# Kernel tuning notes

Measured on AMD Instinct MI355X. Metric: run time of the kernel, lower is better.

Reference implementation:

```python
import jax, jax.numpy as jnp
import numpy as np

N_NODES = 100000
N_EDGES = 1000000
D_IN = 64
D_OUT = 64


def setup_inputs() -> dict:
    key = jax.random.key(0)
    k1, k2, k3, k4, k5 = jax.random.split(key, 5)
    x = jax.random.normal(k1, (N_NODES, D_IN), dtype=jnp.float32)
    W = jax.random.normal(k2, (D_OUT, D_IN), dtype=jnp.float32) / np.sqrt(D_IN)
    edge_weights = jax.random.uniform(k3, (N_EDGES,), dtype=jnp.float32)
    source = jax.random.randint(k4, (N_EDGES,), 0, N_NODES, dtype=jnp.int64 if jax.config.read('jax_enable_x64') else jnp.int32)
    target = jax.random.randint(k5, (N_EDGES,), 0, N_NODES, dtype=jnp.int64 if jax.config.read('jax_enable_x64') else jnp.int32)
    return {"x": x, "W": W, "edge_weights": edge_weights,
            "source": source, "target": target, "num_nodes": N_NODES}


def reference(x, W, edge_weights, source, target, num_nodes):
    # Linear (no bias): h = x @ W^T, shape (num_nodes, out)
    h = jnp.einsum('nd,od->no', x, W)
    # Gather messages per edge, scale by edge weights
    msg = h[source] * edge_weights[:, None]  # (num_edges, out)
    # Scatter-add by target node (sum aggregation)
    delta = jax.ops.segment_sum(msg, target, num_segments=num_nodes)
    return delta
```

## Files before the change

### kernel.cpp

```cpp
#include <hip/hip_runtime.h>


#define D     64
#define BKT   64
#define BSH   6
#define NBMAX 2048
#define CAP   1024
#define CAPB  1024

__global__ __launch_bounds__(256) void gcn_scatter_kernel(
    const float* __restrict__ x, const float* __restrict__ ew,
    const int* __restrict__ src, const int* __restrict__ tgt,
    float* __restrict__ s, int n_edges)
{
    int lane = threadIdx.x & 63;
    int e = blockIdx.x * 4 + (threadIdx.x >> 6);
    if (e >= n_edges) return;
    int sn = src[e];
    int tn = tgt[e];
    float w = ew[e];
    float v = x[(size_t)sn * D + lane] * w;
    atomicAdd(&s[(size_t)tn * D + lane], v);
}

__global__ __launch_bounds__(256) void gcn_gemm_kernel(
    const float* __restrict__ s, const float* __restrict__ W,
    float* __restrict__ out, int n_nodes)
{
    __shared__ float4 xs[64 * 17];
    const int tid  = threadIdx.x;
    const int lane = tid & 63;
    const int wid  = __builtin_amdgcn_readfirstlane(tid >> 6);
    const int row0 = blockIdx.x * 64;

    const float4* s4 = reinterpret_cast<const float4*>(s);
#pragma unroll
    for (int k = 0; k < 4; ++k) {
        int f  = tid + k * 256;
        int r  = f >> 4;
        int c4 = f & 15;
        float4 v = make_float4(0.f, 0.f, 0.f, 0.f);
        if (row0 + r < n_nodes)
            v = s4[(size_t)(row0 + r) * 16 + c4];
        xs[r * 17 + c4] = v;
    }
    __syncthreads();

    float acc[16];
#pragma unroll
    for (int j = 0; j < 16; ++j) acc[j] = 0.f;

    const int o0 = wid * 16;
    const float4* W4 = reinterpret_cast<const float4*>(W);
#pragma unroll
    for (int d4 = 0; d4 < 16; ++d4) {
        float4 xv = xs[lane * 17 + d4];
#pragma unroll
        for (int j = 0; j < 16; ++j) {
            float4 wv = W4[(size_t)(o0 + j) * 16 + d4];
            acc[j] += xv.x * wv.x + xv.y * wv.y + xv.z * wv.z + xv.w * wv.w;
        }
    }

    const int row = row0 + lane;
    if (row < n_nodes) {
        float4* out4 = reinterpret_cast<float4*>(out);
#pragma unroll
        for (int j4 = 0; j4 < 4; ++j4) {
            float4 v = make_float4(acc[j4 * 4 + 0], acc[j4 * 4 + 1],
                                   acc[j4 * 4 + 2], acc[j4 * 4 + 3]);
            out4[(size_t)row * 16 + wid * 4 + j4] = v;
        }
    }
}

__device__ __forceinline__ unsigned f2bf(float f) {
    unsigned u = __float_as_uint(f);
    return (u + 0x7FFFu + ((u >> 16) & 1u)) >> 16;
}

__global__ __launch_bounds__(256) void convert_init_kernel(
    const float* __restrict__ x, uint2* __restrict__ xb, int n4,
    int* __restrict__ bbeg, int* __restrict__ bcur, int nb)
{
    const int g = blockIdx.x * 256 + threadIdx.x;
    if (g < nb) { bbeg[g] = g * CAPB; bcur[g] = g * CAPB; }
    const float4* x4 = reinterpret_cast<const float4*>(x);
    for (int i = g; i < n4; i += gridDim.x * 256) {
        float4 v = x4[i];
        uint2 o;
        o.x = f2bf(v.x) | (f2bf(v.y) << 16);
        o.y = f2bf(v.z) | (f2bf(v.w) << 16);
        xb[i] = o;
    }
}

__global__ __launch_bounds__(256) void convert_hist_kernel(
    const float* __restrict__ x, uint2* __restrict__ xb, int n4,
    const int* __restrict__ tgt, int* __restrict__ bcnt,
    int n_edges, int nb, int epb)
{
    __shared__ int h[NBMAX];
    const int tid = threadIdx.x;
    for (int i = tid; i < nb; i += 256) h[i] = 0;

    const float4* x4 = reinterpret_cast<const float4*>(x);
    for (int i = blockIdx.x * 256 + tid; i < n4; i += gridDim.x * 256) {
        float4 v = x4[i];
        uint2 o;
        o.x = f2bf(v.x) | (f2bf(v.y) << 16);
        o.y = f2bf(v.z) | (f2bf(v.w) << 16);
        xb[i] = o;
    }
    __syncthreads();

    const int e0 = blockIdx.x * epb;
    const int e1 = min(e0 + epb, n_edges);
    for (int e = e0 + tid; e < e1; e += 256)
        atomicAdd(&h[tgt[e] >> BSH], 1);
    __syncthreads();
    for (int b = tid; b < nb; b += 256) {
        int c = h[b];
        if (c) atomicAdd(&bcnt[b], c);
    }
}

__global__ __launch_bounds__(1024) void bucket_scan_kernel(
    const int* __restrict__ bcnt, int* __restrict__ bstarts,
    int* __restrict__ bcur, int nb, int n_edges)
{
    __shared__ int lds[1024];
    const int tid = threadIdx.x;
    const int i0 = 2 * tid, i1 = 2 * tid + 1;
    int v0 = (i0 < nb) ? bcnt[i0] : 0;
    int v1 = (i1 < nb) ? bcnt[i1] : 0;
    int tsum = v0 + v1;
    lds[tid] = tsum;
    __syncthreads();
    for (int off = 1; off < 1024; off <<= 1) {
        int a = (tid >= off) ? lds[tid - off] : 0;
        __syncthreads();
        lds[tid] += a;
        __syncthreads();
    }
    int pre = lds[tid] - tsum;
    if (i0 < nb) { bstarts[i0] = pre;      bcur[i0] = pre; }
    if (i1 < nb) { bstarts[i1] = pre + v0; bcur[i1] = pre + v0; }
    if (tid == 0) bstarts[nb] = n_edges;
}

__global__ __launch_bounds__(256) void bucket_scatter_kernel(
    const int* __restrict__ src, const int* __restrict__ tgt,
    const float* __restrict__ ew, int* __restrict__ bcur,
    int2* __restrict__ pairs, int n_edges, int nb, int epb)
{
    __shared__ int h[NBMAX];
    __shared__ int base[NBMAX];
    const int tid = threadIdx.x;
    for (int i = tid; i < nb; i += 256) h[i] = 0;
    __syncthreads();
    const int e0 = blockIdx.x * epb;
    const int e1 = min(e0 + epb, n_edges);

    for (int e = e0 + tid; e < e1; e += 256)
        atomicAdd(&h[tgt[e] >> BSH], 1);
    __syncthreads();

    for (int b = tid; b < nb; b += 256) {
        int c = h[b];
        base[b] = c ? atomicAdd(&bcur[b], c) : 0;
        h[b] = 0;
    }
    __syncthreads();

    for (int e = e0 + tid; e < e1; e += 256) {
        int t = tgt[e];
        int b = t >> BSH;
        int r = atomicAdd(&h[b], 1);
        pairs[base[b] + r] =
            make_int2(((t & (BKT - 1)) << 24) | src[e], __float_as_int(ew[e]));
    }
}

__global__ __launch_bounds__(512, 6) void bucket_sort_reduce_gemm_kernel(
    const uint2* __restrict__ xb, const float* __restrict__ W,
    const int* __restrict__ bbeg, const int* __restrict__ bend,
    const int2* __restrict__ pairs,
    float* __restrict__ out, int n_nodes, int nb)
{
    __shared__ float Wl[64 * 66];
    __shared__ int2  ep[CAP];
    __shared__ int   segIncl[BKT];
    __shared__ int   rankc[BKT];
    __shared__ float accRow[8][64];

    const int tid  = threadIdx.x;
    const int lane = tid & 63;
    const int wv   = tid >> 6;
    const int q4   = lane >> 4;
    const int m    = lane & 15;

    for (int i = tid; i < 64 * 64; i += 512)
        Wl[(i >> 6) * 66 + (i & 63)] = W[i];

    const int b   = blockIdx.x;
    const int beg = bbeg[b];
    const int end = bend[b];

    float4 acc[8];
#pragma unroll
    for (int s = 0; s < 8; ++s) acc[s] = make_float4(0.f, 0.f, 0.f, 0.f);

    for (int cbeg = beg; cbeg < end; cbeg += CAP) {
        const int ccnt = min(CAP, end - cbeg);

        int2 pr0 = make_int2(0, 0), pr1 = make_int2(0, 0);
        if (tid < ccnt)       pr0 = pairs[cbeg + tid];
        if (tid + 512 < ccnt) pr1 = pairs[cbeg + tid + 512];

        if (tid < BKT) segIncl[tid] = 0;
        __syncthreads();

        if (tid < ccnt)       atomicAdd(&segIncl[((unsigned)pr0.x) >> 24], 1);
        if (tid + 512 < ccnt) atomicAdd(&segIncl[((unsigned)pr1.x) >> 24], 1);
        __syncthreads();

        if (wv == 0) {
            int c0 = segIncl[lane];
            int v = c0;
#pragma unroll
            for (int off = 1; off < 64; off <<= 1) {
                int n = __shfl_up(v, off);
                if (lane >= off) v += n;
            }
            segIncl[lane] = v;
            rankc[lane]   = v - c0;
        }
        __syncthreads();

        if (tid < ccnt) {
            int pos = atomicAdd(&rankc[((unsigned)pr0.x) >> 24], 1);
            ep[pos] = pr0;
        }
        if (tid + 512 < ccnt) {
            int pos = atomicAdd(&rankc[((unsigned)pr1.x) >> 24], 1);
            ep[pos] = pr1;
        }
        __syncthreads();

#pragma unroll
        for (int g = 0; g < 2; ++g) {
            int e0, e1, e2, e3, x1_0, x1_1, x1_2, x1_3;
            {
                const int tl0 = (g * 4 + 0) * 8 + wv;
                const int tl1 = (g * 4 + 1) * 8 + wv;
                const int tl2 = (g * 4 + 2) * 8 + wv;
                const int tl3 = (g * 4 + 3) * 8 + wv;
                e0 = __builtin_amdgcn_readfirstlane(tl0 ? segIncl[tl0 - 1] : 0);
                e1 = __builtin_amdgcn_readfirstlane(segIncl[tl1 - 1]);
                e2 = __builtin_amdgcn_readfirstlane(segIncl[tl2 - 1]);
                e3 = __builtin_amdgcn_readfirstlane(segIncl[tl3 - 1]);
                x1_0 = __builtin_amdgcn_readfirstlane(segIncl[tl0]);
                x1_1 = __builtin_amdgcn_readfirstlane(segIncl[tl1]);
                x1_2 = __builtin_amdgcn_readfirstlane(segIncl[tl2]);
                x1_3 = __builtin_amdgcn_readfirstlane(segIncl[tl3]);
            }
            const int c1_0 = max(x1_0 - 1, 0);
            const int c1_1 = max(x1_1 - 1, 0);
            const int c1_2 = max(x1_2 - 1, 0);
            const int c1_3 = max(x1_3 - 1, 0);
            float4 a0 = acc[g * 4 + 0];
            float4 a1 = acc[g * 4 + 1];
            float4 a2 = acc[g * 4 + 2];
            float4 a3 = acc[g * 4 + 3];

            while ((e0 < x1_0) | (e1 < x1_1) | (e2 < x1_2) | (e3 < x1_3)) {
                const int ea0 = e0 + q4, ea1 = e1 + q4;
                const int ea2 = e2 + q4, ea3 = e3 + q4;
                int2 p0 = ep[min(ea0, c1_0)];
                int2 p1 = ep[min(ea1, c1_1)];
                int2 p2 = ep[min(ea2, c1_2)];
                int2 p3 = ep[min(ea3, c1_3)];
                uint2 r0 = xb[(size_t)(p0.x & 0xFFFFFF) * 16 + m];
                uint2 r1 = xb[(size_t)(p1.x & 0xFFFFFF) * 16 + m];
                uint2 r2 = xb[(size_t)(p2.x & 0xFFFFFF) * 16 + m];
                uint2 r3 = xb[(size_t)(p3.x & 0xFFFFFF) * 16 + m];
                float w0 = (ea0 < x1_0) ? __int_as_float(p0.y) : 0.f;
                float w1 = (ea1 < x1_1) ? __int_as_float(p1.y) : 0.f;
                float w2 = (ea2 < x1_2) ? __int_as_float(p2.y) : 0.f;
                float w3 = (ea3 < x1_3) ? __int_as_float(p3.y) : 0.f;
                a0.x += w0 * __uint_as_float(r0.x << 16);
                a0.y += w0 * __uint_as_float(r0.x & 0xFFFF0000u);
                a0.z += w0 * __uint_as_float(r0.y << 16);
                a0.w += w0 * __uint_as_float(r0.y & 0xFFFF0000u);
                a1.x += w1 * __uint_as_float(r1.x << 16);
                a1.y += w1 * __uint_as_float(r1.x & 0xFFFF0000u);
                a1.z += w1 * __uint_as_float(r1.y << 16);
                a1.w += w1 * __uint_as_float(r1.y & 0xFFFF0000u);
                a2.x += w2 * __uint_as_float(r2.x << 16);
                a2.y += w2 * __uint_as_float(r2.x & 0xFFFF0000u);
                a2.z += w2 * __uint_as_float(r2.y << 16);
                a2.w += w2 * __uint_as_float(r2.y & 0xFFFF0000u);
                a3.x += w3 * __uint_as_float(r3.x << 16);
                a3.y += w3 * __uint_as_float(r3.x & 0xFFFF0000u);
                a3.z += w3 * __uint_as_float(r3.y << 16);
                a3.w += w3 * __uint_as_float(r3.y & 0xFFFF0000u);
                e0 += 4; e1 += 4; e2 += 4; e3 += 4;
            }
            acc[g * 4 + 0] = a0;
            acc[g * 4 + 1] = a1;
            acc[g * 4 + 2] = a2;
            acc[g * 4 + 3] = a3;
        }
        __syncthreads();
    }

    const int node0 = b * BKT;
#pragma unroll
    for (int s = 0; s < 8; ++s) {
        const int node = node0 + s * 8 + wv;
        if (node < n_nodes) {
            float4 a = acc[s];
            a.x += __shfl_xor(a.x, 16); a.y += __shfl_xor(a.y, 16);
            a.z += __shfl_xor(a.z, 16); a.w += __shfl_xor(a.w, 16);
            a.x += __shfl_xor(a.x, 32); a.y += __shfl_xor(a.y, 32);
            a.z += __shfl_xor(a.z, 32); a.w += __shfl_xor(a.w, 32);
            if (lane < 16)
                *reinterpret_cast<float4*>(&accRow[wv][m * 4]) = a;
            asm volatile("s_waitcnt lgkmcnt(0)" ::: "memory");

            float o = 0.f;
            const float2* a2p = reinterpret_cast<const float2*>(&accRow[wv][0]);
            const float2* w2p = reinterpret_cast<const float2*>(&Wl[lane * 66]);
#pragma unroll
            for (int d2 = 0; d2 < 32; ++d2) {
                float2 aq = a2p[d2];
                float2 wq = w2p[d2];
                o += aq.x * wq.x + aq.y * wq.y;
            }
            out[(size_t)node * D + lane] = o;
            asm volatile("s_waitcnt lgkmcnt(0)" ::: "memory");
        }
    }
}

extern "C" void kernel_launch(void* const* d_in, const int* in_sizes, int n_in,
                              void* d_out, int out_size, void* d_ws, size_t ws_size,
                              hipStream_t stream)
{
    const float* x   = (const float*)d_in[0];
    const float* W   = (const float*)d_in[1];
    const float* ew  = (const float*)d_in[2];
    const int*   src = (const int*)d_in[3];
    const int*   tgt = (const int*)d_in[4];

    const int n_nodes = in_sizes[0] / D;
    const int n_edges = in_sizes[2];
    const int nb = (n_nodes + BKT - 1) / BKT;
    const int cblocks = 256;
    const int epbC = (n_edges + cblocks - 1) / cblocks;

    {
        int*   bcur  = (int*)d_ws;
        int*   bbeg  = bcur + nb;
        size_t ints  = 2 * (size_t)nb;
        ints = (ints + 1) & ~(size_t)1;
        int2*  pairs = (int2*)((int*)d_ws + ints);
        uint2* xb    = (uint2*)(pairs + (size_t)nb * CAPB);
        const size_t need = ints * 4 + (size_t)nb * CAPB * 8 +
                            (size_t)n_nodes * 128;

        if (nb <= NBMAX && n_nodes <= (1 << 24) && ws_size >= need) {
            convert_init_kernel<<<256, 256, 0, stream>>>(
                x, xb, n_nodes * 16, bbeg, bcur, nb);
            bucket_scatter_kernel<<<cblocks, 256, 0, stream>>>(
                src, tgt, ew, bcur, pairs, n_edges, nb, epbC);
            bucket_sort_reduce_gemm_kernel<<<nb, 512, 0, stream>>>(
                xb, W, bbeg, bcur, pairs, (float*)d_out, n_nodes, nb);
            return;
        }
    }

    {
        int*   bcnt    = (int*)d_ws;
        int*   bstarts = bcnt + NBMAX;
        int*   bcur    = bstarts + NBMAX + 1;
        size_t ints    = 3 * (size_t)NBMAX + 1;
        ints = (ints + 1) & ~(size_t)1;
        int2*  pairs   = (int2*)((int*)d_ws + ints);
        uint2* xb      = (uint2*)(pairs + n_edges);
        const size_t need = ints * 4 + (size_t)n_edges * 8 +
                            (size_t)n_nodes * 128;

        if (nb <= NBMAX && n_nodes <= (1 << 24) && ws_size >= need) {
            hipMemsetAsync(bcnt, 0, (size_t)nb * sizeof(int), stream);
            const int ablocks = 256;
            const int epbA = (n_edges + ablocks - 1) / ablocks;
            convert_hist_kernel<<<ablocks, 256, 0, stream>>>(
                x, xb, n_nodes * 16, tgt, bcnt, n_edges, nb, epbA);
            bucket_scan_kernel<<<1, 1024, 0, stream>>>(bcnt, bstarts, bcur,
                                                       nb, n_edges);
            bucket_scatter_kernel<<<cblocks, 256, 0, stream>>>(
                src, tgt, ew, bcur, pairs, n_edges, nb, epbC);
            bucket_sort_reduce_gemm_kernel<<<nb, 512, 0, stream>>>(
                xb, W, bstarts, bstarts + 1, pairs, (float*)d_out, n_nodes, nb);
            return;
        }
    }

    float* s = (float*)d_ws;
    hipMemsetAsync(s, 0, (size_t)n_nodes * D * sizeof(float), stream);
    gcn_scatter_kernel<<<(n_edges + 3) / 4, 256, 0, stream>>>(x, ew, src, tgt, s, n_edges);
    gcn_gemm_kernel<<<(n_nodes + 63) / 64, 256, 0, stream>>>(s, W, (float*)d_out, n_nodes);
}
```

Baseline: 112.4 us.

## Fuse bf16 conversion and bucket scatter into one heterogeneous prep kernel

```diff
diff --git a/kernel.cpp b/kernel.cpp
--- a/kernel.cpp
+++ b/kernel.cpp
@@ -7,6 +7,8 @@
 #define NBMAX 2048
 #define CAP   1024
 #define CAPB  1024
+#define SCAT_BLOCKS 256
+#define CONV_BLOCKS 256
 
 __global__ __launch_bounds__(256) void gcn_scatter_kernel(
     const float* __restrict__ x, const float* __restrict__ ew,
@@ -79,19 +81,51 @@
     return (u + 0x7FFFu + ((u >> 16) & 1u)) >> 16;
 }
 
-__global__ __launch_bounds__(256) void convert_init_kernel(
+__global__ __launch_bounds__(256) void fat_prep_kernel(
     const float* __restrict__ x, uint2* __restrict__ xb, int n4,
-    int* __restrict__ bbeg, int* __restrict__ bcur, int nb)
-{
-    const int g = blockIdx.x * 256 + threadIdx.x;
-    if (g < nb) { bbeg[g] = g * CAPB; bcur[g] = g * CAPB; }
-    const float4* x4 = reinterpret_cast<const float4*>(x);
-    for (int i = g; i < n4; i += gridDim.x * 256) {
-        float4 v = x4[i];
-        uint2 o;
-        o.x = f2bf(v.x) | (f2bf(v.y) << 16);
-        o.y = f2bf(v.z) | (f2bf(v.w) << 16);
-        xb[i] = o;
+    const int* __restrict__ src, const int* __restrict__ tgt,
+    const float* __restrict__ ew, int* __restrict__ bcnt,
+    int2* __restrict__ pairs, int n_edges, int nb, int epb)
+{
+    const int tid = threadIdx.x;
+
+    if (blockIdx.x >= SCAT_BLOCKS) {
+        const int cb = blockIdx.x - SCAT_BLOCKS;
+        const float4* x4 = reinterpret_cast<const float4*>(x);
+        for (int i = cb * 256 + tid; i < n4; i += CONV_BLOCKS * 256) {
+            float4 v = x4[i];
+            uint2 o;
+            o.x = f2bf(v.x) | (f2bf(v.y) << 16);
+            o.y = f2bf(v.z) | (f2bf(v.w) << 16);
+            xb[i] = o;
+        }
+        return;
+    }
+
+    __shared__ int h[NBMAX];
+    __shared__ int base[NBMAX];
+    for (int i = tid; i < nb; i += 256) h[i] = 0;
+    __syncthreads();
+    const int e0 = blockIdx.x * epb;
+    const int e1 = min(e0 + epb, n_edges);
+
+    for (int e = e0 + tid; e < e1; e += 256)
+        atomicAdd(&h[tgt[e] >> BSH], 1);
+    __syncthreads();
+
+    for (int b = tid; b < nb; b += 256) {
+        int c = h[b];
+        base[b] = c ? (b * CAPB + atomicAdd(&bcnt[b], c)) : 0;
+        h[b] = 0;
+    }
+    __syncthreads();
+
+    for (int e = e0 + tid; e < e1; e += 256) {
+        int t = tgt[e];
+        int b = t >> BSH;
+        int r = atomicAdd(&h[b], 1);
+        pairs[base[b] + r] =
+            make_int2(((t & (BKT - 1)) << 24) | src[e], __float_as_int(ew[e]));
     }
 }
 
@@ -186,7 +220,7 @@
     const uint2* __restrict__ xb, const float* __restrict__ W,
     const int* __restrict__ bbeg, const int* __restrict__ bend,
     const int2* __restrict__ pairs,
-    float* __restrict__ out, int n_nodes, int nb)
+    float* __restrict__ out, int n_nodes, int nb, int capb)
 {
     __shared__ float Wl[64 * 66];
     __shared__ int2  ep[CAP];
@@ -204,8 +238,8 @@
         Wl[(i >> 6) * 66 + (i & 63)] = W[i];
 
     const int b   = blockIdx.x;
-    const int beg = bbeg[b];
-    const int end = bend[b];
+    const int beg = capb ? b * capb : bbeg[b];
+    const int end = capb ? beg + bend[b] : bend[b];
 
     float4 acc[8];
 #pragma unroll
@@ -357,26 +391,23 @@
     const int n_nodes = in_sizes[0] / D;
     const int n_edges = in_sizes[2];
     const int nb = (n_nodes + BKT - 1) / BKT;
-    const int cblocks = 256;
-    const int epbC = (n_edges + cblocks - 1) / cblocks;
+    const int epbS = (n_edges + SCAT_BLOCKS - 1) / SCAT_BLOCKS;
 
     {
-        int*   bcur  = (int*)d_ws;
-        int*   bbeg  = bcur + nb;
-        size_t ints  = 2 * (size_t)nb;
-        ints = (ints + 1) & ~(size_t)1;
+        int*   bcnt  = (int*)d_ws;
+        size_t ints  = ((size_t)nb + 1) & ~(size_t)1;
         int2*  pairs = (int2*)((int*)d_ws + ints);
         uint2* xb    = (uint2*)(pairs + (size_t)nb * CAPB);
         const size_t need = ints * 4 + (size_t)nb * CAPB * 8 +
                             (size_t)n_nodes * 128;
 
         if (nb <= NBMAX && n_nodes <= (1 << 24) && ws_size >= need) {
-            convert_init_kernel<<<256, 256, 0, stream>>>(
-                x, xb, n_nodes * 16, bbeg, bcur, nb);
-            bucket_scatter_kernel<<<cblocks, 256, 0, stream>>>(
-                src, tgt, ew, bcur, pairs, n_edges, nb, epbC);
+            hipMemsetAsync(bcnt, 0, (size_t)nb * sizeof(int), stream);
+            fat_prep_kernel<<<SCAT_BLOCKS + CONV_BLOCKS, 256, 0, stream>>>(
+                x, xb, n_nodes * 16, src, tgt, ew, bcnt, pairs,
+                n_edges, nb, epbS);
             bucket_sort_reduce_gemm_kernel<<<nb, 512, 0, stream>>>(
-                xb, W, bbeg, bcur, pairs, (float*)d_out, n_nodes, nb);
+                xb, W, bcnt, bcnt, pairs, (float*)d_out, n_nodes, nb, CAPB);
             return;
         }
     }
@@ -400,10 +431,12 @@
                 x, xb, n_nodes * 16, tgt, bcnt, n_edges, nb, epbA);
             bucket_scan_kernel<<<1, 1024, 0, stream>>>(bcnt, bstarts, bcur,
                                                        nb, n_edges);
-            bucket_scatter_kernel<<<cblocks, 256, 0, stream>>>(
-                src, tgt, ew, bcur, pairs, n_edges, nb, epbC);
+            bucket_scatter_kernel<<<256, 256, 0, stream>>>(
+                src, tgt, ew, bcur, pairs, n_edges, nb,
+                (n_edges + 255) / 256);
             bucket_sort_reduce_gemm_kernel<<<nb, 512, 0, stream>>>(
-                xb, W, bstarts, bstarts + 1, pairs, (float*)d_out, n_nodes, nb);
+                xb, W, bstarts, bstarts + 1, pairs, (float*)d_out,
+                n_nodes, nb, 0);
             return;
         }
     }
```

Result: faster. 110.2 us, median of 2 (-2.0%).
